# Performance work log

Measured on AMD Instinct MI355X. Metric: run time of the kernel, lower is better.

## Reference

```python
import jax, jax.numpy as jnp
import numpy as np

B, S = 256, 512
MEM, DK, DV, DS = 32, 128, 128, 256
NQ = 10000
ABILITY_SCALE = 3.0


def _kaiming(key, shape, fan_in):
    return jax.random.normal(key, shape, dtype=jnp.float32) * jnp.sqrt(2.0 / fan_in)


def setup_inputs() -> dict:
    key = jax.random.key(0)
    ks = jax.random.split(key, 20)
    q_data = jax.random.randint(ks[0], (B, S), 0, NQ + 1)
    qa_data = jax.random.randint(ks[1], (B, S), 0, 2 * NQ + 1)
    # embedding tables (padding_idx=0 row zeroed)
    q_table = _kaiming(ks[2], (NQ + 1, DK), DK).at[0].set(0.0)
    qa_table = _kaiming(ks[3], (2 * NQ + 1, DV), DV).at[0].set(0.0)
    # DKVMN memories
    key_memory = _kaiming(ks[4], (MEM, DK), DK)
    init_value_memory = _kaiming(ks[5], (MEM, DV), DV)
    # DKVMN write transforms (erase: sigmoid, add: tanh)
    W_erase = _kaiming(ks[6], (DV, DV), DV); b_erase = jnp.zeros((DV,), jnp.float32)
    W_add = _kaiming(ks[7], (DV, DV), DV); b_add = jnp.zeros((DV,), jnp.float32)
    # summary network: Linear(DV+DK -> DS) + tanh
    W_sum = _kaiming(ks[8], (DV + DK, DS), DV + DK); b_sum = jnp.zeros((DS,), jnp.float32)
    # student ability net: Linear(DS->DS)+tanh, Linear(DS->1)
    W_ab1 = _kaiming(ks[9], (DS, DS), DS); b_ab1 = jnp.zeros((DS,), jnp.float32)
    W_ab2 = _kaiming(ks[10], (DS, 1), DS); b_ab2 = jnp.zeros((1,), jnp.float32)
    # item difficulty net: Linear(DK->DK)+tanh, Linear(DK->1)
    W_df1 = _kaiming(ks[11], (DK, DK), DK); b_df1 = jnp.zeros((DK,), jnp.float32)
    W_df2 = _kaiming(ks[12], (DK, 1), DK); b_df2 = jnp.zeros((1,), jnp.float32)
    return dict(q_data=q_data, qa_data=qa_data, q_table=q_table, qa_table=qa_table,
                key_memory=key_memory, init_value_memory=init_value_memory,
                W_erase=W_erase, b_erase=b_erase, W_add=W_add, b_add=b_add,
                W_sum=W_sum, b_sum=b_sum, W_ab1=W_ab1, b_ab1=b_ab1,
                W_ab2=W_ab2, b_ab2=b_ab2, W_df1=W_df1, b_df1=b_df1,
                W_df2=W_df2, b_df2=b_df2)


def _forward(q_data, qa_data, q_table, qa_table, key_memory, init_value_memory,
             W_erase, b_erase, W_add, b_add, W_sum, b_sum,
             W_ab1, b_ab1, W_ab2, b_ab2, W_df1, b_df1, W_df2, b_df2):
    qe = q_table[q_data]            # [B,S,DK]
    qae = qa_table[qa_data]         # [B,S,DV]
    # attention weights for every timestep (depend only on q embeddings)
    w_all = jax.nn.softmax(jnp.einsum('bsd,md->bsm', qe, key_memory), axis=-1)  # [B,S,M]
    erase = jax.nn.sigmoid(qae @ W_erase + b_erase)   # [B,S,DV]
    add = jnp.tanh(qae @ W_add + b_add)               # [B,S,DV]
    Mv0 = jnp.broadcast_to(init_value_memory, (q_data.shape[0], MEM, DV))

    def step(Mv, xs):
        w, e, a = xs  # [B,M], [B,DV], [B,DV]
        read = jnp.einsum('bm,bmd->bd', w, Mv)  # read BEFORE write
        Mv = Mv * (1.0 - w[:, :, None] * e[:, None, :]) + w[:, :, None] * a[:, None, :]
        return Mv, read

    xs = (jnp.swapaxes(w_all, 0, 1), jnp.swapaxes(erase, 0, 1), jnp.swapaxes(add, 0, 1))
    _, reads = jax.lax.scan(step, Mv0, xs)          # reads: [S,B,DV]
    reads = jnp.swapaxes(reads, 0, 1)               # [B,S,DV]

    summary = jnp.tanh(jnp.concatenate([reads, qe], axis=-1) @ W_sum + b_sum)  # [B,S,DS]
    ability = jnp.tanh(summary @ W_ab1 + b_ab1) @ W_ab2 + b_ab2                # [B,S,1]
    difficulty = jnp.tanh(qe @ W_df1 + b_df1) @ W_df2 + b_df2                  # [B,S,1]
    z = ABILITY_SCALE * ability - difficulty
    pred = jax.nn.sigmoid(z)
    return (pred[..., 0], ability[..., 0], difficulty[..., 0], z[..., 0])


def reference(q_data, qa_data, q_table, qa_table, key_memory, init_value_memory,
              W_erase, b_erase, W_add, b_add, W_sum, b_sum,
              W_ab1, b_ab1, W_ab2, b_ab2, W_df1, b_df1, W_df2, b_df2):
    return _forward(q_data, qa_data, q_table, qa_table, key_memory, init_value_memory,
                    W_erase, b_erase, W_add, b_add, W_sum, b_sum,
                    W_ab1, b_ab1, W_ab2, b_ab2, W_df1, b_df1, W_df2, b_df2)
```

## Files before the change

kernel.cpp:

```cpp
#include <hip/hip_runtime.h>
#include <hip/hip_bf16.h>

typedef unsigned short u16;
typedef unsigned int   u32;

#define B_N   256
#define S_N   512
#define BSN   (B_N * S_N)
#define MEMN  32
#define DKN   128
#define DVN   128
#define DSN   256

typedef __attribute__((ext_vector_type(8))) short bf16x8;
typedef __attribute__((ext_vector_type(4))) float f32x4;

__device__ __forceinline__ float bf2f(u16 u) {
  union { u32 i; float f; } v; v.i = ((u32)u) << 16; return v.f;
}
__device__ __forceinline__ u16 f2bf(float f) {
  union { float f; u32 i; } v; v.f = f;
  u32 x = v.i;
  x += 0x7fffu + ((x >> 16) & 1u);
  return (u16)(x >> 16);
}
__device__ __forceinline__ u32 pack2(float a, float b) {
  return (u32)f2bf(a) | ((u32)f2bf(b) << 16);
}
__device__ __forceinline__ float sigmoid_fast(float x) { return 1.f / (1.f + __expf(-x)); }
__device__ __forceinline__ float tanh_fast(float x)    { return 1.f - 2.f / (__expf(2.f * x) + 1.f); }

#define GLOAD_LDS16(g, l)                                         \
  __builtin_amdgcn_global_load_lds(                               \
      (const __attribute__((address_space(1))) void*)(g),         \
      (__attribute__((address_space(3))) void*)(l), 16, 0, 0)

__global__ __launch_bounds__(256) void kPrep(
    const float* __restrict__ W_sum, const float* __restrict__ W_ab1,
    const float* __restrict__ W_er,  const float* __restrict__ W_ad,
    const float* __restrict__ key_mem, const float* __restrict__ W_df1,
    u16* __restrict__ WsumT, u16* __restrict__ Wab1T,
    u16* __restrict__ WerT,  u16* __restrict__ WaddT,
    u16* __restrict__ BqT)
{
  int e = blockIdx.x * 256 + threadIdx.x;
  if (e < 65536) {
    const int n = e >> 8, k = e & 255;
    WsumT[e] = f2bf(W_sum[k * 256 + n]);
  } else if (e < 131072) {
    e -= 65536;
    const int n = e >> 8, k = e & 255;
    Wab1T[e] = f2bf(W_ab1[k * 256 + n]);
  } else if (e < 147456) {
    e -= 131072;
    const int n = e >> 7, k = e & 127;
    WerT[e] = f2bf(W_er[k * 128 + n]);
  } else if (e < 163840) {
    e -= 147456;
    const int n = e >> 7, k = e & 127;
    WaddT[e] = f2bf(W_ad[k * 128 + n]);
  } else if (e < 184320) {
    e -= 163840;
    const int n = e >> 7, k = e & 127;
    BqT[e] = f2bf(n < 32 ? key_mem[n * 128 + k] : W_df1[k * 128 + (n - 32)]);
  }
}

__global__ __launch_bounds__(256) void kErAdd(
    const int* __restrict__ qa_data, const float* __restrict__ qa_table,
    const u16* __restrict__ WerT, const u16* __restrict__ WaddT,
    const float* __restrict__ b_er, const float* __restrict__ b_ad,
    u16* __restrict__ eras, u16* __restrict__ addb)
{
  __shared__ __align__(16) u16 As[4 * 128 * 32];
  __shared__ __align__(16) u16 Bs[2 * 128 * 32];
  const int tid = threadIdx.x;
  const int p0  = blockIdx.x * 128;

  {
    const int r = tid >> 1, h = tid & 1;
    const long base = (long)qa_data[p0 + r] * DVN + h * 64;
    #pragma unroll
    for (int g = 0; g < 8; ++g) {
      const int k0 = h * 64 + g * 8;
      const float4 fa = *(const float4*)(qa_table + base + g * 8);
      const float4 fb = *(const float4*)(qa_table + base + g * 8 + 4);
      uint4 pk;
      pk.x = pack2(fa.x, fa.y); pk.y = pack2(fa.z, fa.w);
      pk.z = pack2(fb.x, fb.y); pk.w = pack2(fb.z, fb.w);
      *(uint4*)(As + (k0 >> 5) * 4096 + r * 32 + (k0 & 31)) = pk;
    }
  }

  const int lane = tid & 63, wave = tid >> 6;
  const int wr = (wave >> 1) * 64, wc = (wave & 1) * 64;
  const int c15 = lane & 15, q = lane >> 4;

  for (int sel = 0; sel < 2; ++sel) {
    const u16*   Wt = sel ? WaddT : WerT;
    const float* bb = sel ? b_ad  : b_er;
    u16*       outp = sel ? addb  : eras;

    {
      #pragma unroll
      for (int u = 0; u < 2; ++u) {
        const int f = tid + 256 * u;
        const int n = f >> 2, j = f & 3;
        *(uint4*)(Bs + n * 32 + j * 8) = *(const uint4*)(Wt + n * 128 + j * 8);
      }
    }
    __syncthreads();

    f32x4 acc[4][4];
    #pragma unroll
    for (int b = 0; b < 4; ++b) {
      const float bv = bb[wc + 16 * b + c15];
      #pragma unroll
      for (int a = 0; a < 4; ++a) acc[a][b] = (f32x4){bv, bv, bv, bv};
    }

    for (int c = 0; c < 4; ++c) {
      const int cur = c & 1;
      uint4 st[2];
      const bool more = (c + 1 < 4);
      if (more) {
        #pragma unroll
        for (int u = 0; u < 2; ++u) {
          const int f = tid + 256 * u;
          const int n = f >> 2, j = f & 3;
          st[u] = *(const uint4*)(Wt + n * 128 + (c + 1) * 32 + j * 8);
        }
      }
      bf16x8 af[4], bf[4];
      #pragma unroll
      for (int a = 0; a < 4; ++a)
        af[a] = *(const bf16x8*)(As + c * 4096 + (wr + 16 * a + c15) * 32 + q * 8);
      #pragma unroll
      for (int b = 0; b < 4; ++b)
        bf[b] = *(const bf16x8*)(Bs + cur * 4096 + (wc + 16 * b + c15) * 32 + q * 8);
      #pragma unroll
      for (int a = 0; a < 4; ++a)
        #pragma unroll
        for (int b = 0; b < 4; ++b)
          acc[a][b] = __builtin_amdgcn_mfma_f32_16x16x32_bf16(af[a], bf[b], acc[a][b], 0, 0, 0);
      if (more) {
        #pragma unroll
        for (int u = 0; u < 2; ++u) {
          const int f = tid + 256 * u;
          const int n = f >> 2, j = f & 3;
          *(uint4*)(Bs + (cur ^ 1) * 4096 + n * 32 + j * 8) = st[u];
        }
      }
      __syncthreads();
    }

    const int colb = wc + c15;
    #pragma unroll
    for (int a = 0; a < 4; ++a) {
      #pragma unroll
      for (int r = 0; r < 4; ++r) {
        const int row = p0 + wr + 16 * a + 4 * q + r;
        u16* yp = outp + (long)row * DVN + colb;
        #pragma unroll
        for (int b = 0; b < 4; ++b) {
          const float v = sel ? tanh_fast(acc[a][b][r]) : sigmoid_fast(acc[a][b][r]);
          yp[16 * b] = f2bf(v);
        }
      }
    }
  }
}

__global__ __launch_bounds__(256) void kQe(
    const int* __restrict__ q_data, const float* __restrict__ q_table,
    const u16* __restrict__ BqT,
    const float* __restrict__ bdf1, const float* __restrict__ Wdf2,
    const float* __restrict__ bdf2,
    float* __restrict__ w_all, float* __restrict__ diff,
    u16* __restrict__ sin_buf)
{
  __shared__ __align__(16) u16 As[4 * 128 * 32];
  __shared__ __align__(16) u16 Bs[4 * 160 * 32];
  const int tid = threadIdx.x;
  const int p0  = blockIdx.x * 128;

  {
    const int r = tid >> 1, h = tid & 1;
    const long base = (long)q_data[p0 + r] * DKN + h * 64;
    #pragma unroll
    for (int g = 0; g < 8; ++g) {
      const int k0 = h * 64 + g * 8;
      const float4 fa = *(const float4*)(q_table + base + g * 8);
      const float4 fb = *(const float4*)(q_table + base + g * 8 + 4);
      uint4 pk;
      pk.x = pack2(fa.x, fa.y); pk.y = pack2(fa.z, fa.w);
      pk.z = pack2(fb.x, fb.y); pk.w = pack2(fb.z, fb.w);
      *(uint4*)(As + (k0 >> 5) * 4096 + r * 32 + (k0 & 31)) = pk;
      *(uint4*)(sin_buf + (long)(p0 + r) * DSN + DKN + k0) = pk;
    }
  }
  {
    #pragma unroll
    for (int u = 0; u < 10; ++u) {
      const int f = tid + 256 * u;
      const int n = f >> 4, jj = f & 15;
      *(uint4*)(Bs + (jj >> 2) * 5120 + n * 32 + (jj & 3) * 8) =
          *(const uint4*)(BqT + n * 128 + jj * 8);
    }
  }
  __syncthreads();

  const int lane = tid & 63, wave = tid >> 6;
  const int wr = (wave >> 1) * 64, wc = (wave & 1) * 80;
  const int c15 = lane & 15, q = lane >> 4;

  f32x4 acc[4][5];
  float w2v[5];
  #pragma unroll
  for (int b = 0; b < 5; ++b) {
    const int col = wc + 16 * b + c15;
    const float bv = (col < 32) ? 0.f : bdf1[col - 32];
    w2v[b] = (col < 32) ? 0.f : Wdf2[col - 32];
    #pragma unroll
    for (int a = 0; a < 4; ++a) acc[a][b] = (f32x4){bv, bv, bv, bv};
  }

  #pragma unroll
  for (int c = 0; c < 4; ++c) {
    bf16x8 af[4], bf[5];
    #pragma unroll
    for (int a = 0; a < 4; ++a)
      af[a] = *(const bf16x8*)(As + c * 4096 + (wr + 16 * a + c15) * 32 + q * 8);
    #pragma unroll
    for (int b = 0; b < 5; ++b)
      bf[b] = *(const bf16x8*)(Bs + c * 5120 + (wc + 16 * b + c15) * 32 + q * 8);
    #pragma unroll
    for (int a = 0; a < 4; ++a)
      #pragma unroll
      for (int b = 0; b < 5; ++b)
        acc[a][b] = __builtin_amdgcn_mfma_f32_16x16x32_bf16(af[a], bf[b], acc[a][b], 0, 0, 0);
  }

  if (wc == 0) {
    #pragma unroll
    for (int a = 0; a < 4; ++a) {
      #pragma unroll
      for (int r = 0; r < 4; ++r) {
        float s0 = acc[a][0][r], s1 = acc[a][1][r];
        float mx = fmaxf(s0, s1);
        mx = fmaxf(mx, __shfl_xor(mx, 1, 64));
        mx = fmaxf(mx, __shfl_xor(mx, 2, 64));
        mx = fmaxf(mx, __shfl_xor(mx, 4, 64));
        mx = fmaxf(mx, __shfl_xor(mx, 8, 64));
        const float e0 = __expf(s0 - mx), e1 = __expf(s1 - mx);
        float sm = e0 + e1;
        sm += __shfl_xor(sm, 1, 64);
        sm += __shfl_xor(sm, 2, 64);
        sm += __shfl_xor(sm, 4, 64);
        sm += __shfl_xor(sm, 8, 64);
        const float inv = 1.f / sm;
        const int row = p0 + wr + 16 * a + 4 * q + r;
        w_all[(long)row * MEMN + c15]      = e0 * inv;
        w_all[(long)row * MEMN + 16 + c15] = e1 * inv;
      }
    }
  }

  float sv[4][4];
  #pragma unroll
  for (int a = 0; a < 4; ++a) {
    #pragma unroll
    for (int r = 0; r < 4; ++r) {
      float s = 0.f;
      #pragma unroll
      for (int b = 0; b < 5; ++b)
        s = fmaf(tanh_fast(acc[a][b][r]), w2v[b], s);
      s += __shfl_xor(s, 1, 64);
      s += __shfl_xor(s, 2, 64);
      s += __shfl_xor(s, 4, 64);
      s += __shfl_xor(s, 8, 64);
      sv[a][r] = s;
    }
  }
  __syncthreads();
  float* red = (float*)As;
  if ((wave & 1) && c15 == 0) {
    #pragma unroll
    for (int a = 0; a < 4; ++a)
      #pragma unroll
      for (int r = 0; r < 4; ++r)
        red[wr + 16 * a + 4 * q + r] = sv[a][r];
  }
  __syncthreads();
  if (!(wave & 1) && c15 == 0) {
    const float bd = bdf2[0];
    #pragma unroll
    for (int a = 0; a < 4; ++a)
      #pragma unroll
      for (int r = 0; r < 4; ++r) {
        const int rr = wr + 16 * a + 4 * q + r;
        diff[p0 + rr] = sv[a][r] + red[rr] + bd;
      }
  }
}

#define CHUNK_BYTES 12288
#define PB_OFF      25088

#define KSTAGE(K, BUF)                                                        \
  {                                                                           \
    const char* wsrc = (const char*)(w_all + (pbase + (long)(K) * 32) * MEMN);\
    const char* esrc = (const char*)(eras + (pbase + (long)(K) * 32) * DVN)   \
                       + ch * 128;                                            \
    const char* asrc = (const char*)(addb + (pbase + (long)(K) * 32) * DVN)   \
                       + ch * 128;                                            \
    char* dst = lds + (BUF) * CHUNK_BYTES;                                    \
    _Pragma("unroll")                                                         \
    for (int r = 0; r < 3; ++r) {                                             \
      const int o = (tid + r * 256) * 16;                                     \
      const char* src;                                                        \
      if (o < 4096) {                                                         \
        src = wsrc + o;                                                       \
      } else if (o < 8192) {                                                  \
        const int f = o - 4096;                                               \
        src = esrc + (f >> 7) * 256 + (f & 127);                              \
      } else {                                                                \
        const int f = o - 8192;                                               \
        src = asrc + (f >> 7) * 256 + (f & 127);                              \
      }                                                                       \
      GLOAD_LDS16(src, dst + o);                                              \
    }                                                                         \
  }

__global__ __launch_bounds__(256) void kScan(
    const float* __restrict__ w_all, const u16* __restrict__ eras,
    const u16* __restrict__ addb, const float* __restrict__ init_mem,
    u16* __restrict__ sin_buf)
{
  __shared__ __align__(16) char lds[PB_OFF + 32768];
  const int tid = threadIdx.x;
  const int ch  = blockIdx.x & 1;
  const int lc  = tid >> 2;
  const int gc  = ch * 64 + lc;
  const int h   = tid & 3;
  const long pbase = (long)(blockIdx.x >> 1) * S_N;

  float* pb = (float*)(lds + PB_OFF);

  float Mv[8];
  #pragma unroll
  for (int m = 0; m < 8; ++m) Mv[m] = init_mem[(h * 8 + m) * DVN + gc];

  const int lc2  = tid & 63;
  const int sblk = tid >> 6;
  u16* sp2 = sin_buf + pbase * DSN + ch * 64 + lc2;

  KSTAGE(0, 0)
  for (int k = 0; k < 16; ++k) {
    __syncthreads();
    if (k + 1 < 16) KSTAGE(k + 1, (k + 1) & 1)

    const char*  wb  = lds + (k & 1) * CHUNK_BYTES;
    const f32x4* wl4 = (const f32x4*)wb;
    const u16*   el  = (const u16*)(wb + 4096);
    const u16*   al  = (const u16*)(wb + 8192);

    f32x4 Wr[3][2];
    u16 er[3], ar[3];
    #pragma unroll
    for (int i = 0; i < 2; ++i) Wr[0][i] = wl4[h * 2 + i];
    er[0] = el[lc]; ar[0] = al[lc];
    #pragma unroll
    for (int i = 0; i < 2; ++i) Wr[1][i] = wl4[8 + h * 2 + i];
    er[1] = el[64 + lc]; ar[1] = al[64 + lc];

    #pragma unroll
    for (int s = 0; s < 32; ++s) {
      const int cur = s % 3, nx2 = (s + 2) % 3;
      Wr[nx2][0] = wl4[(s + 2) * 8 + h * 2];
      Wr[nx2][1] = wl4[(s + 2) * 8 + h * 2 + 1];
      er[nx2] = el[(s + 2) * 64 + lc];
      ar[nx2] = al[(s + 2) * 64 + lc];
      {
        float ac0 = 0.f, ac1 = 0.f, ac2 = 0.f, ac3 = 0.f;
        #pragma unroll
        for (int i = 0; i < 2; ++i) {
          ac0 = fmaf(Wr[cur][i][0], Mv[4 * i + 0], ac0);
          ac1 = fmaf(Wr[cur][i][1], Mv[4 * i + 1], ac1);
          ac2 = fmaf(Wr[cur][i][2], Mv[4 * i + 2], ac2);
          ac3 = fmaf(Wr[cur][i][3], Mv[4 * i + 3], ac3);
        }
        pb[s * 256 + lc * 4 + h] = (ac0 + ac1) + (ac2 + ac3);
        const float ec = bf2f(er[cur]);
        const float an = -bf2f(ar[cur]);
        #pragma unroll
        for (int i = 0; i < 2; ++i) {
          #pragma unroll
          for (int j = 0; j < 4; ++j) {
            const float t = fmaf(ec, Mv[4 * i + j], an);
            Mv[4 * i + j] = fmaf(-Wr[cur][i][j], t, Mv[4 * i + j]);
          }
        }
      }
    }

    __syncthreads();
    const int lb = k * 32;
    #pragma unroll
    for (int r = 0; r < 8; ++r) {
      const int s = sblk * 8 + r;
      const f32x4 pv = *(const f32x4*)(pb + s * 256 + lc2 * 4);
      sp2[(long)(lb + s) * DSN] = f2bf((pv[0] + pv[1]) + (pv[2] + pv[3]));
    }
  }
}

__global__ __launch_bounds__(256) void kSum(
    const u16* __restrict__ X, const u16* __restrict__ WsumT,
    const float* __restrict__ bias, u16* __restrict__ Y)
{
  __shared__ __align__(16) u16 As[8 * 128 * 32];
  __shared__ __align__(16) u16 Bs[2 * 128 * 32];
  const int tid = threadIdx.x;
  const int p0  = blockIdx.x * 128;
  const int j0  = blockIdx.y * 128;

  {
    #pragma unroll
    for (int u = 0; u < 16; ++u) {
      const int f = tid + 256 * u;
      const int r = f >> 5, j = f & 31;
      const uint4 raw = *(const uint4*)(X + (long)(p0 + r) * DSN + j * 8);
      *(uint4*)(As + (j >> 2) * 4096 + r * 32 + (j & 3) * 8) = raw;
    }
  }
  {
    #pragma unroll
    for (int u = 0; u < 2; ++u) {
      const int f = tid + 256 * u;
      const int n = f >> 2, j = f & 3;
      *(uint4*)(Bs + n * 32 + j * 8) = *(const uint4*)(WsumT + (j0 + n) * 256 + j * 8);
    }
  }
  __syncthreads();

  const int lane = tid & 63, wave = tid >> 6;
  const int wr = (wave >> 1) * 64, wc = (wave & 1) * 64;
  const int c15 = lane & 15, q = lane >> 4;

  f32x4 acc[4][4];
  #pragma unroll
  for (int b = 0; b < 4; ++b) {
    const float bv = bias[j0 + wc + 16 * b + c15];
    #pragma unroll
    for (int a = 0; a < 4; ++a) acc[a][b] = (f32x4){bv, bv, bv, bv};
  }

  for (int c = 0; c < 8; ++c) {
    const int cur = c & 1;
    uint4 st[2];
    const bool more = (c + 1 < 8);
    if (more) {
      #pragma unroll
      for (int u = 0; u < 2; ++u) {
        const int f = tid + 256 * u;
        const int n = f >> 2, j = f & 3;
        st[u] = *(const uint4*)(WsumT + (j0 + n) * 256 + (c + 1) * 32 + j * 8);
      }
    }
    bf16x8 af[4], bf[4];
    #pragma unroll
    for (int a = 0; a < 4; ++a)
      af[a] = *(const bf16x8*)(As + c * 4096 + (wr + 16 * a + c15) * 32 + q * 8);
    #pragma unroll
    for (int b = 0; b < 4; ++b)
      bf[b] = *(const bf16x8*)(Bs + cur * 4096 + (wc + 16 * b + c15) * 32 + q * 8);
    #pragma unroll
    for (int a = 0; a < 4; ++a)
      #pragma unroll
      for (int b = 0; b < 4; ++b)
        acc[a][b] = __builtin_amdgcn_mfma_f32_16x16x32_bf16(af[a], bf[b], acc[a][b], 0, 0, 0);
    if (more) {
      #pragma unroll
      for (int u = 0; u < 2; ++u) {
        const int f = tid + 256 * u;
        const int n = f >> 2, j = f & 3;
        *(uint4*)(Bs + (cur ^ 1) * 4096 + n * 32 + j * 8) = st[u];
      }
    }
    __syncthreads();
  }

  const int colb = j0 + wc + c15;
  #pragma unroll
  for (int a = 0; a < 4; ++a) {
    #pragma unroll
    for (int r = 0; r < 4; ++r) {
      const int row = p0 + wr + 16 * a + 4 * q + r;
      u16* yp = Y + (long)row * DSN + colb;
      #pragma unroll
      for (int b = 0; b < 4; ++b)
        yp[16 * b] = f2bf(tanh_fast(acc[a][b][r]));
    }
  }
}

__global__ __launch_bounds__(256) void kAb(
    const u16* __restrict__ X, const u16* __restrict__ Wab1T,
    const float* __restrict__ bias, const float* __restrict__ Wab2,
    float* __restrict__ part)
{
  __shared__ __align__(16) u16 As[8 * 128 * 32];
  __shared__ __align__(16) u16 Bs[2 * 128 * 32];
  const int tid = threadIdx.x;
  const int p0  = blockIdx.x * 128;
  const int j0  = blockIdx.y * 128;

  {
    #pragma unroll
    for (int u = 0; u < 16; ++u) {
      const int f = tid + 256 * u;
      const int r = f >> 5, j = f & 31;
      const uint4 raw = *(const uint4*)(X + (long)(p0 + r) * DSN + j * 8);
      *(uint4*)(As + (j >> 2) * 4096 + r * 32 + (j & 3) * 8) = raw;
    }
  }
  {
    #pragma unroll
    for (int u = 0; u < 2; ++u) {
      const int f = tid + 256 * u;
      const int n = f >> 2, j = f & 3;
      *(uint4*)(Bs + n * 32 + j * 8) = *(const uint4*)(Wab1T + (j0 + n) * 256 + j * 8);
    }
  }
  __syncthreads();

  const int lane = tid & 63, wave = tid >> 6;
  const int wr = (wave >> 1) * 64, wc = (wave & 1) * 64;
  const int c15 = lane & 15, q = lane >> 4;

  f32x4 acc[4][4];
  float w2v[4];
  #pragma unroll
  for (int b = 0; b < 4; ++b) {
    const int col = j0 + wc + 16 * b + c15;
    const float bv = bias[col];
    w2v[b] = Wab2[col];
    #pragma unroll
    for (int a = 0; a < 4; ++a) acc[a][b] = (f32x4){bv, bv, bv, bv};
  }

  for (int c = 0; c < 8; ++c) {
    const int cur = c & 1;
    uint4 st[2];
    const bool more = (c + 1 < 8);
    if (more) {
      #pragma unroll
      for (int u = 0; u < 2; ++u) {
        const int f = tid + 256 * u;
        const int n = f >> 2, j = f & 3;
        st[u] = *(const uint4*)(Wab1T + (j0 + n) * 256 + (c + 1) * 32 + j * 8);
      }
    }
    bf16x8 af[4], bf[4];
    #pragma unroll
    for (int a = 0; a < 4; ++a)
      af[a] = *(const bf16x8*)(As + c * 4096 + (wr + 16 * a + c15) * 32 + q * 8);
    #pragma unroll
    for (int b = 0; b < 4; ++b)
      bf[b] = *(const bf16x8*)(Bs + cur * 4096 + (wc + 16 * b + c15) * 32 + q * 8);
    #pragma unroll
    for (int a = 0; a < 4; ++a)
      #pragma unroll
      for (int b = 0; b < 4; ++b)
        acc[a][b] = __builtin_amdgcn_mfma_f32_16x16x32_bf16(af[a], bf[b], acc[a][b], 0, 0, 0);
    if (more) {
      #pragma unroll
      for (int u = 0; u < 2; ++u) {
        const int f = tid + 256 * u;
        const int n = f >> 2, j = f & 3;
        *(uint4*)(Bs + (cur ^ 1) * 4096 + n * 32 + j * 8) = st[u];
      }
    }
    __syncthreads();
  }

  float sv[4][4];
  #pragma unroll
  for (int a = 0; a < 4; ++a) {
    #pragma unroll
    for (int r = 0; r < 4; ++r) {
      float s = 0.f;
      #pragma unroll
      for (int b = 0; b < 4; ++b)
        s = fmaf(tanh_fast(acc[a][b][r]), w2v[b], s);
      s += __shfl_xor(s, 1, 64);
      s += __shfl_xor(s, 2, 64);
      s += __shfl_xor(s, 4, 64);
      s += __shfl_xor(s, 8, 64);
      sv[a][r] = s;
    }
  }
  float* red = (float*)Bs;
  if ((wave & 1) && c15 == 0) {
    #pragma unroll
    for (int a = 0; a < 4; ++a)
      #pragma unroll
      for (int r = 0; r < 4; ++r)
        red[wr + 16 * a + 4 * q + r] = sv[a][r];
  }
  __syncthreads();
  if (!(wave & 1) && c15 == 0) {
    #pragma unroll
    for (int a = 0; a < 4; ++a)
      #pragma unroll
      for (int r = 0; r < 4; ++r) {
        const int rr = wr + 16 * a + 4 * q + r;
        part[(long)blockIdx.y * BSN + p0 + rr] = sv[a][r] + red[rr];
      }
  }
}

__global__ __launch_bounds__(256) void kOut(
    const float* __restrict__ part, const float* __restrict__ diff,
    const float* __restrict__ bab2, float* __restrict__ out)
{
  const int p = blockIdx.x * 256 + threadIdx.x;
  const float ab = part[p] + part[BSN + p] + bab2[0];
  const float d  = diff[p];
  const float z  = 3.0f * ab - d;
  out[p]           = sigmoid_fast(z);
  out[BSN + p]     = ab;
  out[2 * BSN + p] = d;
  out[3 * BSN + p] = z;
}

extern "C" void kernel_launch(void* const* d_in, const int* in_sizes, int n_in,
                              void* d_out, int out_size, void* d_ws, size_t ws_size,
                              hipStream_t stream)
{
  const int*   q_data   = (const int*)d_in[0];
  const int*   qa_data  = (const int*)d_in[1];
  const float* q_table  = (const float*)d_in[2];
  const float* qa_table = (const float*)d_in[3];
  const float* key_mem  = (const float*)d_in[4];
  const float* init_mem = (const float*)d_in[5];
  const float* W_erase  = (const float*)d_in[6];
  const float* b_erase  = (const float*)d_in[7];
  const float* W_add    = (const float*)d_in[8];
  const float* b_add    = (const float*)d_in[9];
  const float* W_sum    = (const float*)d_in[10];
  const float* b_sum    = (const float*)d_in[11];
  const float* W_ab1    = (const float*)d_in[12];
  const float* b_ab1    = (const float*)d_in[13];
  const float* W_ab2    = (const float*)d_in[14];
  const float* b_ab2    = (const float*)d_in[15];
  const float* W_df1    = (const float*)d_in[16];
  const float* b_df1    = (const float*)d_in[17];
  const float* W_df2    = (const float*)d_in[18];
  const float* b_df2    = (const float*)d_in[19];

  char* ws = (char*)d_ws;
  float* w_all = (float*)(ws + 0);
  u16*   eras  = (u16*)(ws + 16777216);
  u16*   addb  = (u16*)(ws + 50331648);
  u16*   sinb  = (u16*)(ws + 83886080);
  float* diffb = (float*)(ws + 150994944);
  float* part  = (float*)(ws + 151519232);
  u16*   WerT  = (u16*)(ws + 152567808);
  u16*   WaddT = (u16*)(ws + 152600576);
  u16*   WsumT = (u16*)(ws + 152633344);
  u16*   Wab1T = (u16*)(ws + 152764416);
  u16*   BqT   = (u16*)(ws + 152895488);
  u16*   summ  = eras;

  kPrep<<<dim3(720), 256, 0, stream>>>(W_sum, W_ab1, W_erase, W_add, key_mem, W_df1,
                                       WsumT, Wab1T, WerT, WaddT, BqT);
  kErAdd<<<dim3(BSN / 128), 256, 0, stream>>>(qa_data, qa_table, WerT, WaddT,
                                              b_erase, b_add, eras, addb);
  kQe<<<dim3(BSN / 128), 256, 0, stream>>>(q_data, q_table, BqT, b_df1, W_df2, b_df2,
                                           w_all, diffb, sinb);
  kScan<<<dim3(B_N * 2), 256, 0, stream>>>(w_all, eras, addb, init_mem, sinb);
  kSum<<<dim3(BSN / 128, 2), 256, 0, stream>>>(sinb, WsumT, b_sum, summ);
  kAb<<<dim3(BSN / 128, 2), 256, 0, stream>>>(summ, Wab1T, b_ab1, W_ab2, part);
  kOut<<<dim3(BSN / 256), 256, 0, stream>>>(part, diffb, b_ab2, (float*)d_out);
}
```

Before: 355.0 us.

## Stream A and B tiles via direct global-to-LDS double buffering in GEMMs

```diff
diff --git a/kernel.cpp b/kernel.cpp
--- a/kernel.cpp
+++ b/kernel.cpp
@@ -415,35 +415,28 @@
   }
 }
 
+#define SSTAGE(XP, WP, C, BUF)                                              \
+  {                                                                         \
+    _Pragma("unroll")                                                       \
+    for (int u = 0; u < 2; ++u) {                                           \
+      const int idx = tid + 256 * u;                                        \
+      const int row = idx >> 2, k8 = idx & 3;                               \
+      GLOAD_LDS16(XP + (long)(p0 + row) * DSN + (C) * 32 + k8 * 8,          \
+                  Ls + (BUF) * 8192 + idx * 8);                             \
+      GLOAD_LDS16(WP + (long)(j0 + row) * 256 + (C) * 32 + k8 * 8,          \
+                  Ls + (BUF) * 8192 + 4096 + idx * 8);                      \
+    }                                                                       \
+  }
+
 __global__ __launch_bounds__(256) void kSum(
     const u16* __restrict__ X, const u16* __restrict__ WsumT,
     const float* __restrict__ bias, u16* __restrict__ Y)
 {
-  __shared__ __align__(16) u16 As[8 * 128 * 32];
-  __shared__ __align__(16) u16 Bs[2 * 128 * 32];
+  __shared__ __align__(16) u16 Ls[2 * 8192];
   const int tid = threadIdx.x;
   const int p0  = blockIdx.x * 128;
   const int j0  = blockIdx.y * 128;
 
-  {
-    #pragma unroll
-    for (int u = 0; u < 16; ++u) {
-      const int f = tid + 256 * u;
-      const int r = f >> 5, j = f & 31;
-      const uint4 raw = *(const uint4*)(X + (long)(p0 + r) * DSN + j * 8);
-      *(uint4*)(As + (j >> 2) * 4096 + r * 32 + (j & 3) * 8) = raw;
-    }
-  }
-  {
-    #pragma unroll
-    for (int u = 0; u < 2; ++u) {
-      const int f = tid + 256 * u;
-      const int n = f >> 2, j = f & 3;
-      *(uint4*)(Bs + n * 32 + j * 8) = *(const uint4*)(WsumT + (j0 + n) * 256 + j * 8);
-    }
-  }
-  __syncthreads();
-
   const int lane = tid & 63, wave = tid >> 6;
   const int wr = (wave >> 1) * 64, wc = (wave & 1) * 64;
   const int c15 = lane & 15, q = lane >> 4;
@@ -456,39 +449,25 @@
     for (int a = 0; a < 4; ++a) acc[a][b] = (f32x4){bv, bv, bv, bv};
   }
 
+  SSTAGE(X, WsumT, 0, 0)
   for (int c = 0; c < 8; ++c) {
-    const int cur = c & 1;
-    uint4 st[2];
-    const bool more = (c + 1 < 8);
-    if (more) {
-      #pragma unroll
-      for (int u = 0; u < 2; ++u) {
-        const int f = tid + 256 * u;
-        const int n = f >> 2, j = f & 3;
-        st[u] = *(const uint4*)(WsumT + (j0 + n) * 256 + (c + 1) * 32 + j * 8);
-      }
-    }
+    __syncthreads();
+    if (c + 1 < 8) SSTAGE(X, WsumT, c + 1, (c + 1) & 1)
+
+    const u16* Ab = Ls + (c & 1) * 8192;
+    const u16* Bb = Ab + 4096;
     bf16x8 af[4], bf[4];
     #pragma unroll
     for (int a = 0; a < 4; ++a)
-      af[a] = *(const bf16x8*)(As + c * 4096 + (wr + 16 * a + c15) * 32 + q * 8);
+      af[a] = *(const bf16x8*)(Ab + (wr + 16 * a + c15) * 32 + q * 8);
     #pragma unroll
     for (int b = 0; b < 4; ++b)
-      bf[b] = *(const bf16x8*)(Bs + cur * 4096 + (wc + 16 * b + c15) * 32 + q * 8);
+      bf[b] = *(const bf16x8*)(Bb + (wc + 16 * b + c15) * 32 + q * 8);
     #pragma unroll
     for (int a = 0; a < 4; ++a)
       #pragma unroll
       for (int b = 0; b < 4; ++b)
         acc[a][b] = __builtin_amdgcn_mfma_f32_16x16x32_bf16(af[a], bf[b], acc[a][b], 0, 0, 0);
-    if (more) {
-      #pragma unroll
-      for (int u = 0; u < 2; ++u) {
-        const int f = tid + 256 * u;
-        const int n = f >> 2, j = f & 3;
-        *(uint4*)(Bs + (cur ^ 1) * 4096 + n * 32 + j * 8) = st[u];
-      }
-    }
-    __syncthreads();
   }
 
   const int colb = j0 + wc + c15;
@@ -510,30 +489,10 @@
     const float* __restrict__ bias, const float* __restrict__ Wab2,
     float* __restrict__ part)
 {
-  __shared__ __align__(16) u16 As[8 * 128 * 32];
-  __shared__ __align__(16) u16 Bs[2 * 128 * 32];
+  __shared__ __align__(16) u16 Ls[2 * 8192];
   const int tid = threadIdx.x;
   const int p0  = blockIdx.x * 128;
   const int j0  = blockIdx.y * 128;
-
-  {
-    #pragma unroll
-    for (int u = 0; u < 16; ++u) {
-      const int f = tid + 256 * u;
-      const int r = f >> 5, j = f & 31;
-      const uint4 raw = *(const uint4*)(X + (long)(p0 + r) * DSN + j * 8);
-      *(uint4*)(As + (j >> 2) * 4096 + r * 32 + (j & 3) * 8) = raw;
-    }
-  }
-  {
-    #pragma unroll
-    for (int u = 0; u < 2; ++u) {
-      const int f = tid + 256 * u;
-      const int n = f >> 2, j = f & 3;
-      *(uint4*)(Bs + n * 32 + j * 8) = *(const uint4*)(Wab1T + (j0 + n) * 256 + j * 8);
-    }
-  }
-  __syncthreads();
 
   const int lane = tid & 63, wave = tid >> 6;
   const int wr = (wave >> 1) * 64, wc = (wave & 1) * 64;
@@ -550,39 +509,25 @@
     for (int a = 0; a < 4; ++a) acc[a][b] = (f32x4){bv, bv, bv, bv};
   }
 
+  SSTAGE(X, Wab1T, 0, 0)
   for (int c = 0; c < 8; ++c) {
-    const int cur = c & 1;
-    uint4 st[2];
-    const bool more = (c + 1 < 8);
-    if (more) {
-      #pragma unroll
-      for (int u = 0; u < 2; ++u) {
-        const int f = tid + 256 * u;
-        const int n = f >> 2, j = f & 3;
-        st[u] = *(const uint4*)(Wab1T + (j0 + n) * 256 + (c + 1) * 32 + j * 8);
-      }
-    }
+    __syncthreads();
+    if (c + 1 < 8) SSTAGE(X, Wab1T, c + 1, (c + 1) & 1)
+
+    const u16* Ab = Ls + (c & 1) * 8192;
+    const u16* Bb = Ab + 4096;
     bf16x8 af[4], bf[4];
     #pragma unroll
     for (int a = 0; a < 4; ++a)
-      af[a] = *(const bf16x8*)(As + c * 4096 + (wr + 16 * a + c15) * 32 + q * 8);
+      af[a] = *(const bf16x8*)(Ab + (wr + 16 * a + c15) * 32 + q * 8);
     #pragma unroll
     for (int b = 0; b < 4; ++b)
-      bf[b] = *(const bf16x8*)(Bs + cur * 4096 + (wc + 16 * b + c15) * 32 + q * 8);
+      bf[b] = *(const bf16x8*)(Bb + (wc + 16 * b + c15) * 32 + q * 8);
     #pragma unroll
     for (int a = 0; a < 4; ++a)
       #pragma unroll
       for (int b = 0; b < 4; ++b)
         acc[a][b] = __builtin_amdgcn_mfma_f32_16x16x32_bf16(af[a], bf[b], acc[a][b], 0, 0, 0);
-    if (more) {
-      #pragma unroll
-      for (int u = 0; u < 2; ++u) {
-        const int f = tid + 256 * u;
-        const int n = f >> 2, j = f & 3;
-        *(uint4*)(Bs + (cur ^ 1) * 4096 + n * 32 + j * 8) = st[u];
-      }
-    }
-    __syncthreads();
   }
 
   float sv[4][4];
@@ -601,7 +546,8 @@
       sv[a][r] = s;
     }
   }
-  float* red = (float*)Bs;
+  __syncthreads();
+  float* red = (float*)Ls;
   if ((wave & 1) && c15 == 0) {
     #pragma unroll
     for (int a = 0; a < 4; ++a)
```

Result: faster. 327.2 us (-7.9%).
